# Kernel tuning notes

Hardware: AMD Instinct MI355X
Metric: run time of the kernel (lower is better)

## Reference

```python
import jax, jax.numpy as jnp
import numpy as np
from jax import lax

N = 50000
E = 320000
IN_DIM = 128
OUT_DIM = 64
N_CHANNEL = 8
KERNEL = 3
N_REL = 500
BN_EPS = 1e-5


def setup_inputs() -> dict:
    key = jax.random.key(0)
    ks = jax.random.split(key, 10)
    inp = jax.random.normal(ks[0], (N, IN_DIM), dtype=jnp.float32)
    heads = jax.random.randint(ks[1], (E,), 0, N)
    rels = jax.random.randint(ks[2], (E,), 0, N_REL)
    tails = jax.random.randint(ks[3], (E,), 0, N)
    triple = jnp.stack([heads, rels, tails], axis=1).astype(jnp.int64)
    # parameters
    limit_W = float(np.sqrt(6.0 / (IN_DIM + OUT_DIM)))  # xavier_uniform
    W = jax.random.uniform(ks[4], (IN_DIM, OUT_DIM), minval=-limit_W, maxval=limit_W, dtype=jnp.float32)
    rel_embed = jax.random.normal(ks[5], (N_REL, OUT_DIM), dtype=jnp.float32)
    fan_in = 1 * KERNEL * KERNEL
    b = float(1.0 / np.sqrt(fan_in))
    conv_w = jax.random.uniform(ks[6], (N_CHANNEL, 1, KERNEL, KERNEL), minval=-b, maxval=b, dtype=jnp.float32)
    conv_b = jax.random.uniform(ks[7], (N_CHANNEL,), minval=-b, maxval=b, dtype=jnp.float32)
    fc_in = N_CHANNEL * (OUT_DIM - KERNEL + 1) * (3 - KERNEL + 1)
    bf = float(1.0 / np.sqrt(fc_in))
    fc_w = jax.random.uniform(ks[8], (1, fc_in), minval=-bf, maxval=bf, dtype=jnp.float32)
    bn1_gamma = jnp.ones((1,), jnp.float32)
    bn1_beta = jnp.zeros((1,), jnp.float32)
    bn2_gamma = jnp.ones((N_CHANNEL,), jnp.float32)
    bn2_beta = jnp.zeros((N_CHANNEL,), jnp.float32)
    return {"input": inp, "triple": triple, "W": W, "rel_embed": rel_embed,
            "conv_w": conv_w, "conv_b": conv_b, "fc_w": fc_w,
            "bn1_gamma": bn1_gamma, "bn1_beta": bn1_beta,
            "bn2_gamma": bn2_gamma, "bn2_beta": bn2_beta}


def _bn_eval(x, gamma, beta):
    # eval-mode BatchNorm with running_mean=0, running_var=1
    scale = gamma / jnp.sqrt(1.0 + BN_EPS)
    return x * scale.reshape(1, -1, 1, 1) + beta.reshape(1, -1, 1, 1)


def reference(input, triple, W, rel_embed, conv_w, conv_b, fc_w,
              bn1_gamma, bn1_beta, bn2_gamma, bn2_beta):
    n = input.shape[0]
    inp = input @ W                       # [N, out_dim]
    head = triple[:, 0]
    tail = triple[:, 2]
    h = inp[head]                         # [E, D]
    r = rel_embed[triple[:, 1]]           # [E, D]
    t = inp[tail]                         # [E, D]
    # energy function: [E,1,D,3] -> bn1 -> conv -> bn2 -> relu -> fc
    x = jnp.stack([h, r, t], axis=-1)[:, None, :, :]   # [E,1,D,3]
    x = _bn_eval(x, bn1_gamma, bn1_beta)
    y = lax.conv_general_dilated(x, conv_w, (1, 1), 'VALID',
                                 dimension_numbers=('NCHW', 'OIHW', 'NCHW'))
    y = y + conv_b.reshape(1, -1, 1, 1)                 # [E,C,D-2,1]
    y = jax.nn.relu(_bn_eval(y, bn2_gamma, bn2_beta))
    y = y.reshape(y.shape[0], -1)
    e = y @ fc_w[0]                                     # [E]
    e = jax.nn.leaky_relu(e, 0.01)
    # sparse softmax over rows (head) then sparse mm with input_
    m = jax.ops.segment_max(e, head, num_segments=n)
    ex = jnp.exp(e - m[head])
    denom = jax.ops.segment_sum(ex, head, num_segments=n)
    attn = ex / denom[head]
    agg = jax.ops.segment_sum(attn[:, None] * t, head, num_segments=n)
    return jax.nn.elu(agg + inp)
```

## Files before the change

kernel.cpp:

```cpp
#include <hip/hip_runtime.h>
#include <hip/hip_bf16.h>
#include <stdint.h>

#define IN_DIM   128
#define OUT_DIM  64
#define NCH      8
#define N_REL    500
#define BN_EPS   1e-5f
#define CAP      32


#define KEEP(x) asm volatile("" : "+v"(x))

__device__ __forceinline__ float dpp_shl1(float x) {
    return __int_as_float(__builtin_amdgcn_update_dpp(
        0, __float_as_int(x), 0x130, 0xf, 0xf, true));
}

__device__ __forceinline__ float sget(float x) {
    return __int_as_float(__builtin_amdgcn_readfirstlane(__float_as_int(x)));
}

__device__ __forceinline__ void fold_cw_thread(
    const float* __restrict__ conv_w, const float* __restrict__ conv_b,
    const float* __restrict__ bn1g, const float* __restrict__ bn1b,
    const float* __restrict__ bn2g, const float* __restrict__ bn2b,
    float* __restrict__ cw, int c)
{
    if (c >= NCH) return;
    float rs  = rsqrtf(1.f + BN_EPS);
    float s1  = bn1g[0] * rs;
    float be1 = bn1b[0];
    float s2  = bn2g[c] * rs;
    float k1  = s1 * s2;
    float wsum = 0.f;
    for (int d = 0; d < 3; ++d) {
        float a  = conv_w[c * 9 + d * 3 + 0];
        float b  = conv_w[c * 9 + d * 3 + 1];
        float cc = conv_w[c * 9 + d * 3 + 2];
        wsum += a + b + cc;
        cw[c * 3 + d]      = k1 * a;
        cw[24 + c * 3 + d] = k1 * b;
        cw[48 + c * 3 + d] = k1 * cc;
    }
    cw[72 + c] = (be1 * wsum + conv_b[c]) * s2 + bn2b[c];
}

__global__ __launch_bounds__(256) void k_gemm(
    const float* __restrict__ X, const float* __restrict__ W,
    float* __restrict__ inp, int N)
{
    __shared__ float Wl[IN_DIM * OUT_DIM];
    __shared__ float At[64 * IN_DIM];

    const int rows0 = blockIdx.x * 64;
    const float4* W4 = (const float4*)W;
    for (int i = threadIdx.x; i < IN_DIM * OUT_DIM / 4; i += 256)
        ((float4*)Wl)[i] = W4[i];
    for (int i = threadIdx.x; i < 64 * IN_DIM / 4; i += 256) {
        int r  = i >> 5;
        int k4 = i & 31;
        int rr = rows0 + r;
        float4 v = make_float4(0.f, 0.f, 0.f, 0.f);
        if (rr < N) v = ((const float4*)X)[(unsigned)rr * (IN_DIM / 4) + k4];
        int rsw = r ^ ((k4 & 7) << 2);
        At[(k4 * 4 + 0) * 64 + rsw] = v.x;
        At[(k4 * 4 + 1) * 64 + rsw] = v.y;
        At[(k4 * 4 + 2) * 64 + rsw] = v.z;
        At[(k4 * 4 + 3) * 64 + rsw] = v.w;
    }
    __syncthreads();

    const int tx = threadIdx.x & 15;
    const int ty = threadIdx.x >> 4;
    float a00=0.f,a01=0.f,a02=0.f,a03=0.f;
    float a10=0.f,a11=0.f,a12=0.f,a13=0.f;
    float a20=0.f,a21=0.f,a22=0.f,a23=0.f;
    float a30=0.f,a31=0.f,a32=0.f,a33=0.f;

    #pragma unroll 8
    for (int k = 0; k < IN_DIM; ++k) {
        const float4 a = *(const float4*)&At[k * 64 + ((ty * 4) ^ (((k >> 2) & 7) << 2))];
        const float4 b = *(const float4*)&Wl[k * 64 + tx * 4];
        a00 = fmaf(a.x, b.x, a00); a01 = fmaf(a.x, b.y, a01);
        a02 = fmaf(a.x, b.z, a02); a03 = fmaf(a.x, b.w, a03);
        a10 = fmaf(a.y, b.x, a10); a11 = fmaf(a.y, b.y, a11);
        a12 = fmaf(a.y, b.z, a12); a13 = fmaf(a.y, b.w, a13);
        a20 = fmaf(a.z, b.x, a20); a21 = fmaf(a.z, b.y, a21);
        a22 = fmaf(a.z, b.z, a22); a23 = fmaf(a.z, b.w, a23);
        a30 = fmaf(a.w, b.x, a30); a31 = fmaf(a.w, b.y, a31);
        a32 = fmaf(a.w, b.z, a32); a33 = fmaf(a.w, b.w, a33);
    }

    {
        int rr = rows0 + ty * 4 + 0;
        if (rr < N) *(float4*)&inp[(unsigned)rr * OUT_DIM + tx * 4] = make_float4(a00, a01, a02, a03);
        rr = rows0 + ty * 4 + 1;
        if (rr < N) *(float4*)&inp[(unsigned)rr * OUT_DIM + tx * 4] = make_float4(a10, a11, a12, a13);
        rr = rows0 + ty * 4 + 2;
        if (rr < N) *(float4*)&inp[(unsigned)rr * OUT_DIM + tx * 4] = make_float4(a20, a21, a22, a23);
        rr = rows0 + ty * 4 + 3;
        if (rr < N) *(float4*)&inp[(unsigned)rr * OUT_DIM + tx * 4] = make_float4(a30, a31, a32, a33);
    }
}

__global__ __launch_bounds__(256) void k_aux(
    const int* __restrict__ triple, const float* __restrict__ rel_embed,
    const float* __restrict__ conv_w, const float* __restrict__ conv_b,
    const float* __restrict__ bn1g, const float* __restrict__ bn1b,
    const float* __restrict__ bn2g, const float* __restrict__ bn2b,
    int* __restrict__ cnt, unsigned* __restrict__ rtp,
    float* __restrict__ cw, float* __restrict__ Rt,
    int E, int N, int nbucket)
{
    if ((int)blockIdx.x < nbucket) {
        const int bb   = blockIdx.x;
        const int gtid = bb * 256 + threadIdx.x;
        if (bb == 0 && threadIdx.x < NCH)
            fold_cw_thread(conv_w, conv_b, bn1g, bn1b, bn2g, bn2b, cw, threadIdx.x);
        if (gtid < E) {
            int j = gtid;
            int h = triple[3 * j], r = triple[3 * j + 1], t = triple[3 * j + 2];
            h = min(max(h, 0), N - 1);
            r = min(max(r, 0), N_REL - 1);
            t = min(max(t, 0), N - 1);
            int pos = atomicAdd(&cnt[h], 1);
            if (pos < CAP) rtp[(unsigned)h * CAP + pos] =
                ((unsigned)r << 16) | (unsigned)t;
        }
    } else {
        const int rb  = blockIdx.x - nbucket;
        const int ln  = threadIdx.x & 63;
        const int rel = rb * 4 + (threadIdx.x >> 6);
        if (rel < N_REL) {
            float rr = rel_embed[(unsigned)rel * OUT_DIM + ln];
            float r1 = dpp_shl1(rr), r2 = dpp_shl1(r1);
            float rs = rsqrtf(1.f + BN_EPS);
            float s1 = bn1g[0] * rs;
            float q[NCH];
            #pragma unroll
            for (int c = 0; c < NCH; ++c) {
                float k1 = s1 * (bn2g[c] * rs);
                float b0 = k1 * conv_w[c * 9 + 1];
                float b1 = k1 * conv_w[c * 9 + 4];
                float b2 = k1 * conv_w[c * 9 + 7];
                q[c] = fmaf(b0, rr, fmaf(b1, r1, b2 * r2));
            }
            float4* dst = (float4*)&Rt[(unsigned)rel * (OUT_DIM * NCH) + ln * NCH];
            dst[0] = make_float4(q[0], q[1], q[2], q[3]);
            dst[1] = make_float4(q[4], q[5], q[6], q[7]);
        }
    }
}

__device__ __forceinline__ float dpp_wave_sum(float x) {
    x += __int_as_float(__builtin_amdgcn_update_dpp(0, __float_as_int(x), 0x111, 0xf, 0xf, true));
    x += __int_as_float(__builtin_amdgcn_update_dpp(0, __float_as_int(x), 0x112, 0xf, 0xf, true));
    x += __int_as_float(__builtin_amdgcn_update_dpp(0, __float_as_int(x), 0x114, 0xf, 0xf, true));
    x += __int_as_float(__builtin_amdgcn_update_dpp(0, __float_as_int(x), 0x118, 0xf, 0xf, true));
    x += __int_as_float(__builtin_amdgcn_update_dpp(0, __float_as_int(x), 0x142, 0xf, 0xf, true));
    x += __int_as_float(__builtin_amdgcn_update_dpp(0, __float_as_int(x), 0x143, 0xf, 0xf, true));
    return __int_as_float(__builtin_amdgcn_readlane(__float_as_int(x), 63));
}

__global__ __launch_bounds__(256) void k_fused_all(
    const float* __restrict__ inp, const float* __restrict__ Rt,
    const float* __restrict__ cw, const float* __restrict__ fc_w,
    const int* __restrict__ cnt, const unsigned* __restrict__ rtp,
    float* __restrict__ out, int N)
{
    const int lane   = threadIdx.x & 63;
    const int wave   = (blockIdx.x * (blockDim.x >> 6)) + (threadIdx.x >> 6);
    const int nwaves = gridDim.x * (blockDim.x >> 6);

    float cA0[NCH], cA1[NCH], cA2[NCH], cC0[NCH], cC1[NCH], cC2[NCH], k0c[NCH];
    #pragma unroll
    for (int c = 0; c < NCH; ++c) {
        cA0[c] = sget(cw[c * 3 + 0]);
        cA1[c] = sget(cw[c * 3 + 1]);
        cA2[c] = sget(cw[c * 3 + 2]);
        cC0[c] = sget(cw[48 + c * 3 + 0]);
        cC1[c] = sget(cw[48 + c * 3 + 1]);
        cC2[c] = sget(cw[48 + c * 3 + 2]);
        k0c[c] = sget(cw[72 + c]);
    }

    float fcl[NCH];
    #pragma unroll
    for (int c = 0; c < NCH; ++c) {
        fcl[c] = (lane < 62) ? fc_w[c * 62 + lane] : 0.f;
        KEEP(fcl[c]);
    }

    for (int h = wave; h < N; h += nwaves) {
        const int deg = min(cnt[h], CAP);

        float h0 = inp[(unsigned)h * OUT_DIM + lane];
        float h1 = dpp_shl1(h0);
        float h2 = dpp_shl1(h1);
        float Ht[NCH];
        #pragma unroll
        for (int c = 0; c < NCH; ++c) {
            float v = k0c[c];
            v = fmaf(cA0[c], h0, v);
            v = fmaf(cA1[c], h1, v);
            v = fmaf(cA2[c], h2, v);
            Ht[c] = v;
            KEEP(Ht[c]);
        }

        float m_run = -INFINITY, l_run = 0.f, agg = 0.f;
        int prt = 0;
        if (lane < deg) prt = (int)rtp[(unsigned)h * CAP + lane];

        if (deg > 0) {
#define LOADE(KK, Q0, Q1, TT)                                                   \
            {   int pk  = __builtin_amdgcn_readlane(prt, (KK));                 \
                int rkL = pk >> 16, tkL = pk & 0xFFFF;                          \
                const float4* qp = (const float4*)&Rt[(unsigned)rkL * (OUT_DIM * NCH) \
                                                      + (unsigned)(lane * NCH)]; \
                Q0 = qp[0]; Q1 = qp[1];                                         \
                TT = inp[(unsigned)tkL * OUT_DIM + lane]; }

#define CHB(c, QC, T0, T1, T2, AX)                                              \
                { float y = Ht[c] + (QC);                                       \
                  y = fmaf(cC0[c], (T0), y);                                    \
                  y = fmaf(cC1[c], (T1), y);                                    \
                  y = fmaf(cC2[c], (T2), y);                                    \
                  AX = fmaf(fmaxf(y, 0.f), fcl[c], AX); }

#define CH8(Q0, Q1, T0, T1, T2, X0, X1)                                         \
                CHB(0, (Q0).x, T0, T1, T2, X0) CHB(1, (Q0).y, T0, T1, T2, X1)   \
                CHB(2, (Q0).z, T0, T1, T2, X0) CHB(3, (Q0).w, T0, T1, T2, X1)   \
                CHB(4, (Q1).x, T0, T1, T2, X0) CHB(5, (Q1).y, T0, T1, T2, X1)   \
                CHB(6, (Q1).z, T0, T1, T2, X0) CHB(7, (Q1).w, T0, T1, T2, X1)

#define SMUPD(S, TT)                                                            \
            {   float ev = fmaxf((S), 0.01f * (S));                             \
                bool  up = ev > m_run;                                          \
                float d  = up ? (m_run - ev) : (ev - m_run);                    \
                float e  = __expf(d);                                           \
                float sc = up ? e : 1.f;                                        \
                float wk = up ? 1.f : e;                                        \
                agg   = fmaf(agg, sc, wk * (TT));                               \
                l_run = fmaf(l_run, sc, wk);                                    \
                m_run = fmaxf(m_run, ev); }

            float4 qa0, qa1, qb0, qb1;
            float  tta, ttb;
            LOADE(0, qa0, qa1, tta)
            LOADE(1, qb0, qb1, ttb)

            int k = 0;
            for (; k + 1 < deg; k += 2) {
                float t1a = dpp_shl1(tta), t2a = dpp_shl1(t1a);
                float t1b = dpp_shl1(ttb), t2b = dpp_shl1(t1b);
                float aA0 = 0.f, aA1 = 0.f, aB0 = 0.f, aB1 = 0.f;
                CH8(qa0, qa1, tta, t1a, t2a, aA0, aA1)
                CH8(qb0, qb1, ttb, t1b, t2b, aB0, aB1)

                float4 nqa0, nqa1, nqb0, nqb1;
                float  nta, ntb;
                LOADE(k + 2, nqa0, nqa1, nta)
                LOADE(k + 3, nqb0, nqb1, ntb)

                float sA = dpp_wave_sum(aA0 + aA1);
                float sB = dpp_wave_sum(aB0 + aB1);

                SMUPD(sA, tta)
                SMUPD(sB, ttb)

                qa0 = nqa0; qa1 = nqa1; qb0 = nqb0; qb1 = nqb1;
                tta = nta;  ttb = ntb;
            }
            if (k < deg) {
                float t1a = dpp_shl1(tta), t2a = dpp_shl1(t1a);
                float aA0 = 0.f, aA1 = 0.f;
                CH8(qa0, qa1, tta, t1a, t2a, aA0, aA1)
                float sA = dpp_wave_sum(aA0 + aA1);
                SMUPD(sA, tta)
            }
#undef SMUPD
#undef CH8
#undef CHB
#undef LOADE
        }
        float aggn = (l_run > 0.f) ? agg / l_run : 0.f;
        float x = aggn + h0;
        float y = x > 0.f ? x : (__expf(x) - 1.f);
        out[(unsigned)h * OUT_DIM + lane] = y;
    }
}

extern "C" void kernel_launch(void* const* d_in, const int* in_sizes, int n_in,
                              void* d_out, int out_size, void* d_ws, size_t ws_size,
                              hipStream_t stream)
{
    const float* input     = (const float*)d_in[0];
    const int*   triple    = (const int*)d_in[1];
    const float* W         = (const float*)d_in[2];
    const float* rel_embed = (const float*)d_in[3];
    const float* conv_w    = (const float*)d_in[4];
    const float* conv_b    = (const float*)d_in[5];
    const float* fc_w      = (const float*)d_in[6];
    const float* bn1g      = (const float*)d_in[7];
    const float* bn1b      = (const float*)d_in[8];
    const float* bn2g      = (const float*)d_in[9];
    const float* bn2b      = (const float*)d_in[10];
    float*       out       = (float*)d_out;

    const int N = in_sizes[0] / IN_DIM;
    const int E = in_sizes[1] / 3;

    auto align = [](size_t x) { return (x + 255) & ~(size_t)255; };
    char* base = (char*)d_ws;
    size_t o = 0;
    float*    inp = (float*)(base + o);    o = align(o + (size_t)N * OUT_DIM * 4);
    unsigned* rtp = (unsigned*)(base + o); o = align(o + (size_t)N * CAP * 4);
    float*    cw  = (float*)(base + o);    o = align(o + 80 * 4);
    int*      cnt = (int*)(base + o);      o = align(o + (size_t)N * 4);
    float*    Rt  = (float*)(base + o);    o = align(o + (size_t)N_REL * OUT_DIM * NCH * 4);

    hipMemsetAsync(cnt, 0, (size_t)N * 4, stream);

    const int nbucket = (E + 255) / 256;
    const int ntab    = (N_REL + 3) / 4;
    k_aux<<<nbucket + ntab, 256, 0, stream>>>(
        triple, rel_embed, conv_w, conv_b, bn1g, bn1b, bn2g, bn2b,
        cnt, rtp, cw, Rt, E, N, nbucket);

    const int ngemm = (N + 63) / 64;
    k_gemm<<<ngemm, 256, 0, stream>>>(input, W, inp, N);

    const int nblk = (N + 3) / 4;
    k_fused_all<<<nblk, 256, 0, stream>>>(inp, Rt, cw, fc_w,
                                          cnt, rtp, out, N);
}
```

Baseline: 182.1 us.

## Merge GEMM and aux kernels into one launch and unroll edge loop by four

The input projection GEMM, the edge bucketing and the relation-table precompute now run as one kernel that splits work by block index, which removes a launch and lets the independent phases overlap. Every block now reserves the GEMM's 64 KB of shared memory even when it only does bucketing, which can lower occupancy for those blocks. The per-node edge loop now handles four edges per iteration with guarded loads and softmax updates, replacing the old two-edge loop with its tail. This adds memory-level parallelism but wastes compute on padded lanes when the degree is not a multiple of four.

```diff
diff --git a/kernel.cpp b/kernel.cpp
--- a/kernel.cpp
+++ b/kernel.cpp
@@ -46,75 +46,71 @@
     cw[72 + c] = (be1 * wsum + conv_b[c]) * s2 + bn2b[c];
 }
 
-__global__ __launch_bounds__(256) void k_gemm(
+__global__ __launch_bounds__(256) void k_build(
     const float* __restrict__ X, const float* __restrict__ W,
-    float* __restrict__ inp, int N)
-{
-    __shared__ float Wl[IN_DIM * OUT_DIM];
-    __shared__ float At[64 * IN_DIM];
-
-    const int rows0 = blockIdx.x * 64;
-    const float4* W4 = (const float4*)W;
-    for (int i = threadIdx.x; i < IN_DIM * OUT_DIM / 4; i += 256)
-        ((float4*)Wl)[i] = W4[i];
-    for (int i = threadIdx.x; i < 64 * IN_DIM / 4; i += 256) {
-        int r  = i >> 5;
-        int k4 = i & 31;
-        int rr = rows0 + r;
-        float4 v = make_float4(0.f, 0.f, 0.f, 0.f);
-        if (rr < N) v = ((const float4*)X)[(unsigned)rr * (IN_DIM / 4) + k4];
-        int rsw = r ^ ((k4 & 7) << 2);
-        At[(k4 * 4 + 0) * 64 + rsw] = v.x;
-        At[(k4 * 4 + 1) * 64 + rsw] = v.y;
-        At[(k4 * 4 + 2) * 64 + rsw] = v.z;
-        At[(k4 * 4 + 3) * 64 + rsw] = v.w;
-    }
-    __syncthreads();
-
-    const int tx = threadIdx.x & 15;
-    const int ty = threadIdx.x >> 4;
-    float a00=0.f,a01=0.f,a02=0.f,a03=0.f;
-    float a10=0.f,a11=0.f,a12=0.f,a13=0.f;
-    float a20=0.f,a21=0.f,a22=0.f,a23=0.f;
-    float a30=0.f,a31=0.f,a32=0.f,a33=0.f;
-
-    #pragma unroll 8
-    for (int k = 0; k < IN_DIM; ++k) {
-        const float4 a = *(const float4*)&At[k * 64 + ((ty * 4) ^ (((k >> 2) & 7) << 2))];
-        const float4 b = *(const float4*)&Wl[k * 64 + tx * 4];
-        a00 = fmaf(a.x, b.x, a00); a01 = fmaf(a.x, b.y, a01);
-        a02 = fmaf(a.x, b.z, a02); a03 = fmaf(a.x, b.w, a03);
-        a10 = fmaf(a.y, b.x, a10); a11 = fmaf(a.y, b.y, a11);
-        a12 = fmaf(a.y, b.z, a12); a13 = fmaf(a.y, b.w, a13);
-        a20 = fmaf(a.z, b.x, a20); a21 = fmaf(a.z, b.y, a21);
-        a22 = fmaf(a.z, b.z, a22); a23 = fmaf(a.z, b.w, a23);
-        a30 = fmaf(a.w, b.x, a30); a31 = fmaf(a.w, b.y, a31);
-        a32 = fmaf(a.w, b.z, a32); a33 = fmaf(a.w, b.w, a33);
-    }
-
-    {
-        int rr = rows0 + ty * 4 + 0;
-        if (rr < N) *(float4*)&inp[(unsigned)rr * OUT_DIM + tx * 4] = make_float4(a00, a01, a02, a03);
-        rr = rows0 + ty * 4 + 1;
-        if (rr < N) *(float4*)&inp[(unsigned)rr * OUT_DIM + tx * 4] = make_float4(a10, a11, a12, a13);
-        rr = rows0 + ty * 4 + 2;
-        if (rr < N) *(float4*)&inp[(unsigned)rr * OUT_DIM + tx * 4] = make_float4(a20, a21, a22, a23);
-        rr = rows0 + ty * 4 + 3;
-        if (rr < N) *(float4*)&inp[(unsigned)rr * OUT_DIM + tx * 4] = make_float4(a30, a31, a32, a33);
-    }
-}
-
-__global__ __launch_bounds__(256) void k_aux(
     const int* __restrict__ triple, const float* __restrict__ rel_embed,
     const float* __restrict__ conv_w, const float* __restrict__ conv_b,
     const float* __restrict__ bn1g, const float* __restrict__ bn1b,
     const float* __restrict__ bn2g, const float* __restrict__ bn2b,
-    int* __restrict__ cnt, unsigned* __restrict__ rtp,
+    float* __restrict__ inp, int* __restrict__ cnt, unsigned* __restrict__ rtp,
     float* __restrict__ cw, float* __restrict__ Rt,
-    int E, int N, int nbucket)
+    int E, int N, int ngemm, int nbucket)
 {
-    if ((int)blockIdx.x < nbucket) {
-        const int bb   = blockIdx.x;
+    __shared__ float Wl[IN_DIM * OUT_DIM];
+    __shared__ float At[64 * IN_DIM];
+
+    if ((int)blockIdx.x < ngemm) {
+        const int rows0 = blockIdx.x * 64;
+        const float4* W4 = (const float4*)W;
+        for (int i = threadIdx.x; i < IN_DIM * OUT_DIM / 4; i += 256)
+            ((float4*)Wl)[i] = W4[i];
+        for (int i = threadIdx.x; i < 64 * IN_DIM / 4; i += 256) {
+            int r  = i >> 5;
+            int k4 = i & 31;
+            int rr = rows0 + r;
+            float4 v = make_float4(0.f, 0.f, 0.f, 0.f);
+            if (rr < N) v = ((const float4*)X)[(unsigned)rr * (IN_DIM / 4) + k4];
+            int rsw = r ^ ((k4 & 7) << 2);
+            At[(k4 * 4 + 0) * 64 + rsw] = v.x;
+            At[(k4 * 4 + 1) * 64 + rsw] = v.y;
+            At[(k4 * 4 + 2) * 64 + rsw] = v.z;
+            At[(k4 * 4 + 3) * 64 + rsw] = v.w;
+        }
+        __syncthreads();
+
+        const int tx = threadIdx.x & 15;
+        const int ty = threadIdx.x >> 4;
+        float a00=0.f,a01=0.f,a02=0.f,a03=0.f;
+        float a10=0.f,a11=0.f,a12=0.f,a13=0.f;
+        float a20=0.f,a21=0.f,a22=0.f,a23=0.f;
+        float a30=0.f,a31=0.f,a32=0.f,a33=0.f;
+
+        #pragma unroll 8
+        for (int k = 0; k < IN_DIM; ++k) {
+            const float4 a = *(const float4*)&At[k * 64 + ((ty * 4) ^ (((k >> 2) & 7) << 2))];
+            const float4 b = *(const float4*)&Wl[k * 64 + tx * 4];
+            a00 = fmaf(a.x, b.x, a00); a01 = fmaf(a.x, b.y, a01);
+            a02 = fmaf(a.x, b.z, a02); a03 = fmaf(a.x, b.w, a03);
+            a10 = fmaf(a.y, b.x, a10); a11 = fmaf(a.y, b.y, a11);
+            a12 = fmaf(a.y, b.z, a12); a13 = fmaf(a.y, b.w, a13);
+            a20 = fmaf(a.z, b.x, a20); a21 = fmaf(a.z, b.y, a21);
+            a22 = fmaf(a.z, b.z, a22); a23 = fmaf(a.z, b.w, a23);
+            a30 = fmaf(a.w, b.x, a30); a31 = fmaf(a.w, b.y, a31);
+            a32 = fmaf(a.w, b.z, a32); a33 = fmaf(a.w, b.w, a33);
+        }
+
+        {
+            int rr = rows0 + ty * 4 + 0;
+            if (rr < N) *(float4*)&inp[(unsigned)rr * OUT_DIM + tx * 4] = make_float4(a00, a01, a02, a03);
+            rr = rows0 + ty * 4 + 1;
+            if (rr < N) *(float4*)&inp[(unsigned)rr * OUT_DIM + tx * 4] = make_float4(a10, a11, a12, a13);
+            rr = rows0 + ty * 4 + 2;
+            if (rr < N) *(float4*)&inp[(unsigned)rr * OUT_DIM + tx * 4] = make_float4(a20, a21, a22, a23);
+            rr = rows0 + ty * 4 + 3;
+            if (rr < N) *(float4*)&inp[(unsigned)rr * OUT_DIM + tx * 4] = make_float4(a30, a31, a32, a33);
+        }
+    } else if ((int)blockIdx.x < ngemm + nbucket) {
+        const int bb   = blockIdx.x - ngemm;
         const int gtid = bb * 256 + threadIdx.x;
         if (bb == 0 && threadIdx.x < NCH)
             fold_cw_thread(conv_w, conv_b, bn1g, bn1b, bn2g, bn2b, cw, threadIdx.x);
@@ -129,7 +125,7 @@
                 ((unsigned)r << 16) | (unsigned)t;
         }
     } else {
-        const int rb  = blockIdx.x - nbucket;
+        const int rb  = blockIdx.x - ngemm - nbucket;
         const int ln  = threadIdx.x & 63;
         const int rel = rb * 4 + (threadIdx.x >> 6);
         if (rel < N_REL) {
@@ -246,39 +242,44 @@
                 l_run = fmaf(l_run, sc, wk);                                    \
                 m_run = fmaxf(m_run, ev); }
 
-            float4 qa0, qa1, qb0, qb1;
-            float  tta, ttb;
-            LOADE(0, qa0, qa1, tta)
-            LOADE(1, qb0, qb1, ttb)
-
-            int k = 0;
-            for (; k + 1 < deg; k += 2) {
-                float t1a = dpp_shl1(tta), t2a = dpp_shl1(t1a);
-                float t1b = dpp_shl1(ttb), t2b = dpp_shl1(t1b);
+            float4 qa0, qa1, qb0, qb1, qc0, qc1, qd0, qd1;
+            float  ta, tb, tc, td;
+            LOADE(0, qa0, qa1, ta)
+            tb = 0.f; tc = 0.f; td = 0.f;
+            qb0 = qa0; qb1 = qa1; qc0 = qa0; qc1 = qa1; qd0 = qa0; qd1 = qa1;
+            if (1 < deg) LOADE(1, qb0, qb1, tb)
+            if (2 < deg) LOADE(2, qc0, qc1, tc)
+            if (3 < deg) LOADE(3, qd0, qd1, td)
+
+            for (int k = 0; k < deg; k += 4) {
+                float t1a = dpp_shl1(ta), t2a = dpp_shl1(t1a);
+                float t1b = dpp_shl1(tb), t2b = dpp_shl1(t1b);
+                float t1c = dpp_shl1(tc), t2c = dpp_shl1(t1c);
+                float t1d = dpp_shl1(td), t2d = dpp_shl1(t1d);
                 float aA0 = 0.f, aA1 = 0.f, aB0 = 0.f, aB1 = 0.f;
-                CH8(qa0, qa1, tta, t1a, t2a, aA0, aA1)
-                CH8(qb0, qb1, ttb, t1b, t2b, aB0, aB1)
-
-                float4 nqa0, nqa1, nqb0, nqb1;
-                float  nta, ntb;
-                LOADE(k + 2, nqa0, nqa1, nta)
-                LOADE(k + 3, nqb0, nqb1, ntb)
+                float aC0 = 0.f, aC1 = 0.f, aD0 = 0.f, aD1 = 0.f;
+                CH8(qa0, qa1, ta, t1a, t2a, aA0, aA1)
+                CH8(qb0, qb1, tb, t1b, t2b, aB0, aB1)
+                CH8(qc0, qc1, tc, t1c, t2c, aC0, aC1)
+                CH8(qd0, qd1, td, t1d, t2d, aD0, aD1)
+
+                float nta = 0.f, ntb = 0.f, ntc = 0.f, ntd = 0.f;
+                if (k + 4 < deg) LOADE(k + 4, qa0, qa1, nta)
+                if (k + 5 < deg) LOADE(k + 5, qb0, qb1, ntb)
+                if (k + 6 < deg) LOADE(k + 6, qc0, qc1, ntc)
+                if (k + 7 < deg) LOADE(k + 7, qd0, qd1, ntd)
 
                 float sA = dpp_wave_sum(aA0 + aA1);
                 float sB = dpp_wave_sum(aB0 + aB1);
-
-                SMUPD(sA, tta)
-                SMUPD(sB, ttb)
-
-                qa0 = nqa0; qa1 = nqa1; qb0 = nqb0; qb1 = nqb1;
-                tta = nta;  ttb = ntb;
-            }
-            if (k < deg) {
-                float t1a = dpp_shl1(tta), t2a = dpp_shl1(t1a);
-                float aA0 = 0.f, aA1 = 0.f;
-                CH8(qa0, qa1, tta, t1a, t2a, aA0, aA1)
-                float sA = dpp_wave_sum(aA0 + aA1);
-                SMUPD(sA, tta)
+                float sC = dpp_wave_sum(aC0 + aC1);
+                float sD = dpp_wave_sum(aD0 + aD1);
+
+                SMUPD(sA, ta)
+                if (k + 1 < deg) SMUPD(sB, tb)
+                if (k + 2 < deg) SMUPD(sC, tc)
+                if (k + 3 < deg) SMUPD(sD, td)
+
+                ta = nta; tb = ntb; tc = ntc; td = ntd;
             }
 #undef SMUPD
 #undef CH8
@@ -323,14 +324,12 @@
 
     hipMemsetAsync(cnt, 0, (size_t)N * 4, stream);
 
+    const int ngemm   = (N + 63) / 64;
     const int nbucket = (E + 255) / 256;
     const int ntab    = (N_REL + 3) / 4;
-    k_aux<<<nbucket + ntab, 256, 0, stream>>>(
-        triple, rel_embed, conv_w, conv_b, bn1g, bn1b, bn2g, bn2b,
-        cnt, rtp, cw, Rt, E, N, nbucket);
-
-    const int ngemm = (N + 63) / 64;
-    k_gemm<<<ngemm, 256, 0, stream>>>(input, W, inp, N);
+    k_build<<<ngemm + nbucket + ntab, 256, 0, stream>>>(
+        input, W, triple, rel_embed, conv_w, conv_b, bn1g, bn1b, bn2g, bn2b,
+        inp, cnt, rtp, cw, Rt, E, N, ngemm, nbucket);
 
     const int nblk = (N + 3) / 4;
     k_fused_all<<<nblk, 256, 0, stream>>>(inp, Rt, cw, fc_w,
```

New measurement: 203.6 us. +11.8%, slower.
